# Performance work log

Hardware: AMD Instinct MI355X
Metric: run time of the kernel (lower is better)

Reference implementation:

```python
import jax, jax.numpy as jnp
import numpy as np

N = 100000; C = 128; H = 8; G = C // 4
B = 2; Z = 40; Y = 996; X = 996
WIN = 12; NUM_WIN = 200; EPS = 1e-3


def _make_indices():
    rng = np.random.RandomState(0)
    total = B * Z * Y * X
    uk = np.unique(rng.randint(0, total, size=300000).astype(np.int64))[:N]
    b = uk // (Z * Y * X); r = uk % (Z * Y * X)
    z = r // (Y * X); r = r % (Y * X)
    y = r // X; x = r % X
    return b, z, y, x, uk


def _neighbors(b, z, y, x, keys, offsets):
    # submanifold conv: output only at active sites; lookup coord+offset in active set
    sk = np.sort(keys); order = np.argsort(keys)
    cols = []
    for dz, dy, dx in offsets:
        nz, ny, nx = z + dz, y + dy, x + dx
        valid = (nz >= 0) & (nz < Z) & (ny >= 0) & (ny < Y) & (nx >= 0) & (nx < X)
        cand = ((b * Z + nz) * Y + ny) * X + nx
        pos = np.searchsorted(sk, cand)
        posc = np.minimum(pos, N - 1)
        found = valid & (sk[posc] == cand)
        cols.append(np.where(found, order[posc], N))  # N = sentinel (zero row)
    return np.stack(cols, axis=1).astype(np.int32)


def setup_inputs() -> dict:
    b, z, y, x, keys = _make_indices()
    off_k = [(dz, dy, dx) for dz in (-1, 0, 1) for dy in (-1, 0, 1) for dx in (-1, 0, 1)]
    off_h = [(0, 0, d) for d in range(-6, 7)]  # kernel (1,1,13) along x
    off_w = [(0, d, 0) for d in range(-6, 7)]  # kernel (1,13,1) along y
    nbr_k = _neighbors(b, z, y, x, keys, off_k)
    nbr_h = _neighbors(b, z, y, x, keys, off_h)
    nbr_w = _neighbors(b, z, y, x, keys, off_w)
    coords = np.stack([y, x], axis=0)
    wis = []
    for d in range(2):
        wkey = b * 1000 + coords[d] // WIN
        _, inv = np.unique(wkey, return_inverse=True)
        wis.append(inv)
    win_inds = np.stack(wis, 0).astype(np.int32)

    ks = jax.random.split(jax.random.key(0), 20)
    s = 0.05
    return dict(
        feats=jax.random.normal(ks[0], (N, C), jnp.float32),
        win_inds=jnp.asarray(win_inds),
        nbr_k=jnp.asarray(nbr_k), nbr_h=jnp.asarray(nbr_h), nbr_w=jnp.asarray(nbr_w),
        bn_g=jnp.ones((2, C)) + s * jax.random.normal(ks[1], (2, C)),
        bn_b=s * jax.random.normal(ks[2], (2, C)),
        Wqkv=s * jax.random.normal(ks[3], (2, C, 3 * C)),
        Wproj=s * jax.random.normal(ks[4], (2, C, C)),
        bproj=s * jax.random.normal(ks[5], (2, C)),
        bn1_g=jnp.ones((2, C)) + s * jax.random.normal(ks[6], (2, C)),
        bn1_b=s * jax.random.normal(ks[7], (2, C)),
        Wk=s * jax.random.normal(ks[8], (2, 27, G, G)),
        Wh=s * jax.random.normal(ks[9], (2, 13, G, G)),
        Ww=s * jax.random.normal(ks[10], (2, 13, G, G)),
        bn2_g=jnp.ones((2, C)) + s * jax.random.normal(ks[11], (2, C)),
        bn2_b=s * jax.random.normal(ks[12], (2, C)),
        fc1_W=s * jax.random.normal(ks[13], (2, C, 2 * C)),
        fc1_b=s * jax.random.normal(ks[14], (2, 2 * C)),
        fc2_W=s * jax.random.normal(ks[15], (2, 2 * C, C)),
        fc2_b=s * jax.random.normal(ks[16], (2, C)),
    )


def _bn(x, g, b):
    # BatchNorm1d, training-mode batch statistics, eps=1e-3
    m = jnp.mean(x, 0)
    v = jnp.var(x, 0)
    return (x - m) * jax.lax.rsqrt(v + EPS) * g + b


def _attn(x, wi, Wqkv, Wp, bp):
    # windowed linear attention: per-window K^T V + normalization by sum(K)
    q, k, v = jnp.split(x @ Wqkv, 3, axis=1)
    q = jax.nn.relu(q).reshape(N, H, C // H)
    k = jax.nn.relu(k).reshape(N, H, C // H)
    v = v.reshape(N, H, C // H)
    kv = jax.ops.segment_sum(jnp.einsum('nhc,nhd->nhcd', k, v), wi, NUM_WIN)
    s = jax.ops.segment_sum(k, wi, NUM_WIN)
    y = jnp.einsum('nhc,nhcd->nhd', q, kv[wi])
    z = jnp.sum(s[wi] * q, -1, keepdims=True)
    y = (y / (z + EPS)).reshape(N, C)
    return y @ Wp + bp


def _subm(f, nbr, W):
    # submanifold sparse conv via precomputed neighbor map (sentinel row = zeros)
    fp = jnp.concatenate([f, jnp.zeros((1, f.shape[1]), f.dtype)], 0)
    return jnp.einsum('nkc,kcd->nd', fp[nbr], W)


def reference(feats, win_inds, nbr_k, nbr_h, nbr_w, bn_g, bn_b, Wqkv, Wproj, bproj,
              bn1_g, bn1_b, Wk, Wh, Ww, bn2_g, bn2_b, fc1_W, fc1_b, fc2_W, fc2_b):
    f = feats
    for d in range(2):  # directions
        x = _attn(_bn(f, bn_g[d], bn_b[d]), win_inds[d], Wqkv[d], Wproj[d], bproj[d])
        f = f + x
        # CWI_FFN_Layer_3D
        fb = _bn(f, bn1_g[d], bn1_b[d])
        f2 = jnp.concatenate([
            _subm(fb[:, :G], nbr_k, Wk[d]),
            _subm(fb[:, G:2 * G], nbr_h, Wh[d]),
            _subm(fb[:, 2 * G:3 * G], nbr_w, Ww[d]),
            fb[:, 3 * G:],
        ], axis=1)
        f = fb + f2
        h = _bn(f, bn2_g[d], bn2_b[d])
        f = f + (jax.nn.relu(h @ fc1_W[d] + fc1_b[d]) @ fc2_W[d] + fc2_b[d])
    return f
```

## Files before the change

### kernel.cpp

```cpp
#include <hip/hip_runtime.h>
#include <math.h>

#define NPTS 100000
#define CCH 128
#define NWIN 200
#define NBLK_STATS 512
#define NBLK_SORT 391
#define SEGSZ 128
#define NSEG_MAX 1024

#define BM 128
#define BN 128
#define BK 64

typedef __attribute__((ext_vector_type(8))) short bf16x8;
typedef __attribute__((ext_vector_type(4))) float f32x4;
typedef __attribute__((ext_vector_type(4))) unsigned short u16x4;

__device__ __forceinline__ unsigned short f2bf(float f) {
    union { float f; unsigned u; } x; x.f = f;
    unsigned r = x.u + 0x7fff + ((x.u >> 16) & 1);
    return (unsigned short)(r >> 16);
}
__device__ __forceinline__ float bf2f(unsigned short h) {
    union { unsigned u; float f; } x; x.u = ((unsigned)h) << 16;
    return x.f;
}

__global__ __launch_bounds__(256) void bn_partial(const float* __restrict__ F,
                                                  float* __restrict__ part) {
    int t = threadIdx.x;
    int b = blockIdx.x;
    int rg = t >> 5;
    int c4 = (t & 31) * 4;
    float s0=0.f,s1=0.f,s2=0.f,s3=0.f,q0=0.f,q1=0.f,q2=0.f,q3=0.f;
    for (int n = b * 8 + rg; n < NPTS; n += NBLK_STATS * 8) {
        float4 v = *reinterpret_cast<const float4*>(&F[(size_t)n * CCH + c4]);
        s0 += v.x; s1 += v.y; s2 += v.z; s3 += v.w;
        q0 += v.x*v.x; q1 += v.y*v.y; q2 += v.z*v.z; q3 += v.w*v.w;
    }
    __shared__ float red[8][256];
    red[rg][c4+0] = s0; red[rg][c4+1] = s1; red[rg][c4+2] = s2; red[rg][c4+3] = s3;
    red[rg][128+c4+0] = q0; red[rg][128+c4+1] = q1; red[rg][128+c4+2] = q2; red[rg][128+c4+3] = q3;
    __syncthreads();
    float a = 0.f;
#pragma unroll
    for (int g = 0; g < 8; g++) a += red[g][t];
    part[b * 256 + t] = a;
}

__global__ __launch_bounds__(256) void bnred_k(const float* __restrict__ part,
                                               float* __restrict__ part2) {
    int t = threadIdx.x;
    int i = blockIdx.x;
    float a = 0.f;
#pragma unroll 8
    for (int j = 0; j < 32; j++) a += part[(size_t)(i * 32 + j) * 256 + t];
    part2[i * 256 + t] = a;
}

__global__ void bn_finalize(const float* __restrict__ part2,
                            const float* __restrict__ g, const float* __restrict__ bb,
                            float* __restrict__ scale, float* __restrict__ shift) {
    int c = threadIdx.x;
    double s = 0.0, q = 0.0;
#pragma unroll
    for (int b = 0; b < 16; b++) {
        s += (double)part2[b * 256 + c];
        q += (double)part2[b * 256 + 128 + c];
    }
    double m = s / (double)NPTS;
    double var = q / (double)NPTS - m * m;
    double rstd = 1.0 / sqrt(var + 1e-3);
    float sc = (float)rstd * g[c];
    scale[c] = sc;
    shift[c] = bb[c] - (float)m * sc;
}

__global__ __launch_bounds__(128) void wprep(
    const float* __restrict__ W, int K, int N,
    const float* __restrict__ sc, const float* __restrict__ sh,
    const float* __restrict__ bias,
    unsigned short* __restrict__ WT, float* __restrict__ biasf)
{
    int n = blockIdx.x;
    int t = threadIdx.x;
    float part = 0.f;
    for (int k = t; k < K; k += 128) {
        float w = W[(size_t)k * N + n];
        float s = sc ? sc[k] * w : w;
        WT[(size_t)n * K + k] = f2bf(s);
        if (sh) part += sh[k] * w;
    }
    __shared__ float red[128];
    red[t] = part;
    __syncthreads();
    for (int o = 64; o > 0; o >>= 1) {
        if (t < o) red[t] += red[t + o];
        __syncthreads();
    }
    if (t == 0) biasf[n] = red[0] + (bias ? bias[n] : 0.f);
}

__global__ void wconv_prep_all(const float* __restrict__ Wk, const float* __restrict__ Wh,
                               const float* __restrict__ Ww, unsigned short* __restrict__ WB) {
    int i = blockIdx.x * 256 + threadIdx.x;
    if (i >= 53 * 1024) return;
    int tap = i >> 10; int rem = i & 1023; int dd = rem >> 5; int c = rem & 31;
    const float* src; int lt;
    if (tap < 27)      { src = Wk; lt = tap; }
    else if (tap < 40) { src = Wh; lt = tap - 27; }
    else               { src = Ww; lt = tap - 40; }
    WB[i] = f2bf(src[lt * 1024 + c * 32 + dd]);
}

template<int NT>
__global__ __launch_bounds__(256) void gemm_knt(
    const float* __restrict__ A, int lda,
    const unsigned short* __restrict__ WT, const float* __restrict__ biasf,
    unsigned short* __restrict__ Out, int ldo, int reluLim)
{
    __shared__ __align__(16) char smem[49664];
    unsigned short* As = (unsigned short*)smem;
    unsigned short* Bs = (unsigned short*)(smem + 32768);
    float* Ep = (float*)(smem + 32768);

    const int tid  = threadIdx.x;
    const int wave = tid >> 6;
    const int lane = tid & 63;
    const int bm = blockIdx.x * BM;
    const int lrow = lane & 15;
    const int lhk  = lane >> 4;

#pragma unroll
    for (int pass = 0; pass < 16; pass++) {
        int row = pass * 8 + (tid >> 5);
        int grow = bm + row;
        int c4 = (tid & 31) * 4;
        float4 v = make_float4(0.f, 0.f, 0.f, 0.f);
        if (grow < NPTS)
            v = *reinterpret_cast<const float4*>(&A[(size_t)grow * lda + c4]);
        u16x4 h4 = { f2bf(v.x), f2bf(v.y), f2bf(v.z), f2bf(v.w) };
        int half = c4 >> 6;
        int cw = c4 & 63;
        int sw = (cw >> 3) ^ (row & 7);
        *reinterpret_cast<u16x4*>(&As[row * 128 + half * 64 + sw * 8 + (cw & 7)]) = h4;
    }

    for (int nt = 0; nt < NT; nt++) {
        const int bn = nt * BN;
        f32x4 acc[2][8];
#pragma unroll
        for (int i = 0; i < 2; i++)
#pragma unroll
            for (int j = 0; j < 8; j++)
                acc[i][j] = (f32x4){0.f, 0.f, 0.f, 0.f};

#pragma unroll
        for (int h = 0; h < 2; h++) {
            __syncthreads();
#pragma unroll
            for (int pass = 0; pass < 4; pass++) {
                int n = pass * 32 + (tid >> 3);
                bf16x8 w = *reinterpret_cast<const bf16x8*>(
                    &WT[(size_t)(bn + n) * 128 + h * 64 + (tid & 7) * 8]);
                int sw = (tid & 7) ^ (n & 7);
                *reinterpret_cast<bf16x8*>(&Bs[n * 64 + sw * 8]) = w;
            }
            __syncthreads();
#pragma unroll
            for (int ks = 0; ks < 2; ks++) {
                bf16x8 af[2], bfr[8];
#pragma unroll
                for (int fi = 0; fi < 2; fi++) {
                    int row = wave * 32 + fi * 16 + lrow;
                    int sw = (ks * 4 + lhk) ^ (row & 7);
                    af[fi] = *reinterpret_cast<const bf16x8*>(&As[row * 128 + h * 64 + sw * 8]);
                }
#pragma unroll
                for (int fj = 0; fj < 8; fj++) {
                    int col = fj * 16 + lrow;
                    int sw = (ks * 4 + lhk) ^ (col & 7);
                    bfr[fj] = *reinterpret_cast<const bf16x8*>(&Bs[col * 64 + sw * 8]);
                }
#pragma unroll
                for (int fi = 0; fi < 2; fi++)
#pragma unroll
                    for (int fj = 0; fj < 8; fj++)
                        acc[fi][fj] = __builtin_amdgcn_mfma_f32_16x16x32_bf16(
                            af[fi], bfr[fj], acc[fi][fj], 0, 0, 0);
            }
        }
        __syncthreads();

#pragma unroll
        for (int ch = 0; ch < 4; ch++) {
            if (wave == ch) {
#pragma unroll
                for (int fi = 0; fi < 2; fi++)
#pragma unroll
                    for (int fj = 0; fj < 8; fj++) {
                        int r0 = fi * 16 + lhk * 4;
                        int col = fj * 16 + lrow;
#pragma unroll
                        for (int r = 0; r < 4; r++)
                            Ep[(r0 + r) * 132 + col] = acc[fi][fj][r];
                    }
            }
            __syncthreads();
#pragma unroll
            for (int pass = 0; pass < 4; pass++) {
                int idx = pass * 256 + tid;
                int r = idx >> 5;
                int c4 = (idx & 31) * 4;
                int rr = bm + ch * 32 + r;
                if (rr < NPTS) {
                    float4 v = *reinterpret_cast<const float4*>(&Ep[r * 132 + c4]);
                    float4 b = *reinterpret_cast<const float4*>(&biasf[bn + c4]);
                    v.x += b.x; v.y += b.y; v.z += b.z; v.w += b.w;
                    int col = bn + c4;
                    if (col + 0 < reluLim) v.x = fmaxf(v.x, 0.f);
                    if (col + 1 < reluLim) v.y = fmaxf(v.y, 0.f);
                    if (col + 2 < reluLim) v.z = fmaxf(v.z, 0.f);
                    if (col + 3 < reluLim) v.w = fmaxf(v.w, 0.f);
                    u16x4 hv = { f2bf(v.x), f2bf(v.y), f2bf(v.z), f2bf(v.w) };
                    *reinterpret_cast<u16x4*>(&Out[(size_t)rr * ldo + bn + c4]) = hv;
                }
            }
            __syncthreads();
        }
    }
}

template<int ABF, int OBF>
__global__ __launch_bounds__(256) void gemm_t(
    const void* __restrict__ Ap, int lda,
    const unsigned short* __restrict__ WT, const float* __restrict__ biasf,
    int K,
    void* __restrict__ Outp, int ldo,
    int reluLim, int addFlag)
{
    __shared__ __align__(16) char smem[34048];
    unsigned short* As = (unsigned short*)smem;
    unsigned short* Bs = As + BM * BK;
    float* Ep = (float*)smem;

    const int tid  = threadIdx.x;
    const int wave = tid >> 6;
    const int lane = tid & 63;
    const int bm = blockIdx.y * BM;
    const int bn = blockIdx.x * BN;

    f32x4 acc[2][8];
#pragma unroll
    for (int i = 0; i < 2; i++)
#pragma unroll
        for (int j = 0; j < 8; j++)
            acc[i][j] = (f32x4){0.f, 0.f, 0.f, 0.f};

    const int lrow = lane & 15;
    const int lhk  = lane >> 4;

    for (int kk = 0; kk < K; kk += BK) {
        if (ABF) {
            const unsigned short* Ab = (const unsigned short*)Ap;
#pragma unroll
            for (int pass = 0; pass < 4; pass++) {
                int row = pass * 32 + (tid >> 3);
                int grow = bm + row;
                bf16x8 w = (bf16x8){0,0,0,0,0,0,0,0};
                if (grow < NPTS)
                    w = *reinterpret_cast<const bf16x8*>(&Ab[(size_t)grow * lda + kk + (tid & 7) * 8]);
                int sw = (tid & 7) ^ (row & 7);
                *reinterpret_cast<bf16x8*>(&As[row * 64 + sw * 8]) = w;
            }
        } else {
            const float* Af = (const float*)Ap;
            const int arow_t = tid >> 4;
            const int acol   = (tid & 15) * 4;
#pragma unroll
            for (int pass = 0; pass < 8; pass++) {
                int row = pass * 16 + arow_t;
                int grow = bm + row;
                float4 v = make_float4(0.f, 0.f, 0.f, 0.f);
                if (grow < NPTS)
                    v = *reinterpret_cast<const float4*>(&Af[(size_t)grow * lda + kk + acol]);
                u16x4 h = { f2bf(v.x), f2bf(v.y), f2bf(v.z), f2bf(v.w) };
                int s = acol >> 3;
                int sw = s ^ (row & 7);
                *reinterpret_cast<u16x4*>(&As[row * 64 + sw * 8 + (acol & 7)]) = h;
            }
        }
#pragma unroll
        for (int pass = 0; pass < 4; pass++) {
            int n = pass * 32 + (tid >> 3);
            bf16x8 w = *reinterpret_cast<const bf16x8*>(&WT[(size_t)(bn + n) * K + kk + (tid & 7) * 8]);
            int sw = (tid & 7) ^ (n & 7);
            *reinterpret_cast<bf16x8*>(&Bs[n * 64 + sw * 8]) = w;
        }
        __syncthreads();

#pragma unroll
        for (int ks = 0; ks < 2; ks++) {
            bf16x8 af[2], bfr[8];
#pragma unroll
            for (int fi = 0; fi < 2; fi++) {
                int row = wave * 32 + fi * 16 + lrow;
                int sw = (ks * 4 + lhk) ^ (row & 7);
                af[fi] = *reinterpret_cast<const bf16x8*>(&As[row * 64 + sw * 8]);
            }
#pragma unroll
            for (int fj = 0; fj < 8; fj++) {
                int col = fj * 16 + lrow;
                int sw = (ks * 4 + lhk) ^ (col & 7);
                bfr[fj] = *reinterpret_cast<const bf16x8*>(&Bs[col * 64 + sw * 8]);
            }
#pragma unroll
            for (int fi = 0; fi < 2; fi++)
#pragma unroll
                for (int fj = 0; fj < 8; fj++)
                    acc[fi][fj] = __builtin_amdgcn_mfma_f32_16x16x32_bf16(
                        af[fi], bfr[fj], acc[fi][fj], 0, 0, 0);
        }
        __syncthreads();
    }

    for (int hh = 0; hh < 2; hh++) {
        if ((wave >> 1) == hh) {
#pragma unroll
            for (int fi = 0; fi < 2; fi++) {
                int row = (wave & 1) * 32 + fi * 16 + (lane >> 4) * 4;
#pragma unroll
                for (int fj = 0; fj < 8; fj++) {
                    int col = fj * 16 + (lane & 15);
#pragma unroll
                    for (int r = 0; r < 4; r++)
                        Ep[(row + r) * 132 + col] = acc[fi][fj][r];
                }
            }
        }
        __syncthreads();
#pragma unroll
        for (int pass = 0; pass < 8; pass++) {
            int idx = pass * 256 + tid;
            int r = idx >> 5;
            int c4 = (idx & 31) * 4;
            int rr = bm + hh * 64 + r;
            if (rr < NPTS) {
                float4 v = *reinterpret_cast<const float4*>(&Ep[r * 132 + c4]);
                float4 b = *reinterpret_cast<const float4*>(&biasf[bn + c4]);
                v.x += b.x; v.y += b.y; v.z += b.z; v.w += b.w;
                int col = bn + c4;
                if (col + 0 < reluLim) v.x = fmaxf(v.x, 0.f);
                if (col + 1 < reluLim) v.y = fmaxf(v.y, 0.f);
                if (col + 2 < reluLim) v.z = fmaxf(v.z, 0.f);
                if (col + 3 < reluLim) v.w = fmaxf(v.w, 0.f);
                if (OBF) {
                    unsigned short* o = (unsigned short*)Outp + (size_t)rr * ldo + bn + c4;
                    u16x4 hv = { f2bf(v.x), f2bf(v.y), f2bf(v.z), f2bf(v.w) };
                    *reinterpret_cast<u16x4*>(o) = hv;
                } else {
                    float* o = (float*)Outp + (size_t)rr * ldo + bn + c4;
                    if (addFlag) {
                        float4 ov = *reinterpret_cast<const float4*>(o);
                        v.x += ov.x; v.y += ov.y; v.z += ov.z; v.w += ov.w;
                    }
                    *reinterpret_cast<float4*>(o) = v;
                }
            }
        }
        __syncthreads();
    }
}

__global__ __launch_bounds__(256) void hist2_k(const int* __restrict__ wi,
                                               int* __restrict__ BH) {
    __shared__ int h[NWIN];
    int t = threadIdx.x;
    if (t < NWIN) h[t] = 0;
    __syncthreads();
    int n = blockIdx.x * 256 + t;
    if (n < NPTS) atomicAdd(&h[wi[n]], 1);
    __syncthreads();
    if (t < NWIN) BH[blockIdx.x * 256 + t] = h[t];
}

__global__ __launch_bounds__(256) void colscan2_k(const int* __restrict__ BH,
                                                  int* __restrict__ OFFB,
                                                  int* __restrict__ TOT) {
    int w = blockIdx.x;
    int t = threadIdx.x;
    __shared__ int s[512];
    int v0 = (t < NBLK_SORT) ? BH[t * 256 + w] : 0;
    int v1 = (t + 256 < NBLK_SORT) ? BH[(t + 256) * 256 + w] : 0;
    s[t] = v0; s[t + 256] = v1;
    __syncthreads();
#pragma unroll
    for (int off = 1; off < 512; off <<= 1) {
        int a0 = (t >= off) ? s[t - off] : 0;
        int a1 = (t + 256 >= off) ? s[t + 256 - off] : 0;
        __syncthreads();
        s[t] += a0;
        s[t + 256] += a1;
        __syncthreads();
    }
    if (t < NBLK_SORT) OFFB[t * 256 + w] = s[t] - v0;
    if (t + 256 < NBLK_SORT) OFFB[(t + 256) * 256 + w] = s[t + 256] - v1;
    if (t == 0) TOT[w] = s[NBLK_SORT - 1];
}

__global__ __launch_bounds__(256) void meta2_k(const int* __restrict__ TOT,
                                               int* __restrict__ OFFS,
                                               int* __restrict__ SEGW, int* __restrict__ SEGP0,
                                               int* __restrict__ SEGP1, int* __restrict__ SEGBASE) {
    __shared__ int offs[NWIN + 1];
    __shared__ int segc[NWIN];
    int t = threadIdx.x;
    if (t < NWIN) segc[t] = TOT[t];
    __syncthreads();
    if (t == 0) {
        int a = 0;
        for (int w = 0; w < NWIN; w++) { int c = segc[w]; offs[w] = a; a += c; }
        offs[NWIN] = a;
    }
    __syncthreads();
    if (t <= NWIN) OFFS[t] = offs[t];
    if (t < NWIN) segc[t] = (offs[t + 1] - offs[t] + SEGSZ - 1) / SEGSZ;
    __syncthreads();
    if (t == 0) {
        int a = 0;
        for (int i = 0; i < NWIN; i++) { int c = segc[i]; segc[i] = a; SEGBASE[i] = a; a += c; }
        SEGBASE[NWIN] = a;
    }
    __syncthreads();
    if (t < NWIN) {
        int b = segc[t];
        int p0 = offs[t], p1 = offs[t + 1];
        for (int p = p0; p < p1; p += SEGSZ) {
            SEGW[b] = t; SEGP0[b] = p; SEGP1[b] = min(p + SEGSZ, p1); b++;
        }
    }
}

__global__ __launch_bounds__(256) void scatter2_k(const int* __restrict__ wi,
                                                  const int* __restrict__ OFFS,
                                                  const int* __restrict__ OFFB,
                                                  int* __restrict__ list) {
    __shared__ int h[NWIN];
    int t = threadIdx.x;
    if (t < NWIN) h[t] = 0;
    __syncthreads();
    int n = blockIdx.x * 256 + t;
    if (n < NPTS) {
        int w = wi[n];
        int r = atomicAdd(&h[w], 1);
        list[OFFS[w] + OFFB[blockIdx.x * 256 + w] + r] = n;
    }
}

__global__ __launch_bounds__(256) void window_kv_seg(
    const unsigned short* __restrict__ R0bf,
    const int* __restrict__ list,
    const int* __restrict__ SEGP0, const int* __restrict__ SEGP1,
    const int* __restrict__ SEGBASE,
    float* __restrict__ PKV)
{
    int sid = blockIdx.x;
    if (sid >= SEGBASE[NWIN]) return;
    int t = threadIdx.x;
    int p0 = SEGP0[sid], p1 = SEGP1[sid];
    __shared__ float buf[8][256];
    float acc[8] = {0.f,0.f,0.f,0.f,0.f,0.f,0.f,0.f};
    float sa = 0.f;
    int f0 = t * 8;
    int h = f0 >> 8;
    int c = (f0 >> 4) & 15;
    int d0 = f0 & 15;
    const int sr = t >> 5;
    const int c8 = (t & 31) * 8;

    for (int g = p0; g < p1; g += 8) {
        int m = min(8, p1 - g);
        int nj[8];
#pragma unroll
        for (int j = 0; j < 8; j++)
            nj[j] = list[(g + j < p1) ? g + j : p1 - 1];
        __syncthreads();
        {
            const unsigned short* row = &R0bf[(size_t)nj[sr] * 384 + 128];
            bf16x8 hv = *reinterpret_cast<const bf16x8*>(&row[c8]);
            float4 lo = make_float4(bf2f((unsigned short)hv[0]), bf2f((unsigned short)hv[1]),
                                    bf2f((unsigned short)hv[2]), bf2f((unsigned short)hv[3]));
            float4 hi = make_float4(bf2f((unsigned short)hv[4]), bf2f((unsigned short)hv[5]),
                                    bf2f((unsigned short)hv[6]), bf2f((unsigned short)hv[7]));
            *reinterpret_cast<float4*>(&buf[sr][c8]) = lo;
            *reinterpret_cast<float4*>(&buf[sr][c8 + 4]) = hi;
        }
        __syncthreads();
#pragma unroll
        for (int j = 0; j < 8; j++) {
            if (j >= m) break;
            float kc = buf[j][h * 16 + c];
#pragma unroll
            for (int i = 0; i < 8; i++) acc[i] += kc * buf[j][128 + h * 16 + d0 + i];
            if (t < 128) sa += buf[j][t];
        }
    }
    float* out = &PKV[(size_t)sid * 2176];
#pragma unroll
    for (int i = 0; i < 8; i++) out[f0 + i] = acc[i];
    if (t < 128) out[2048 + t] = sa;
}

__global__ __launch_bounds__(256) void kv_reduce(
    const float* __restrict__ PKV, const int* __restrict__ SEGBASE,
    float* __restrict__ KV, float* __restrict__ SB)
{
    int w = blockIdx.x;
    int t = threadIdx.x;
    int s0 = SEGBASE[w], s1 = SEGBASE[w + 1];
    float a[8] = {0.f,0.f,0.f,0.f,0.f,0.f,0.f,0.f};
    float sb = 0.f;
    for (int s = s0; s < s1; s++) {
        const float* p = &PKV[(size_t)s * 2176];
#pragma unroll
        for (int i = 0; i < 8; i++) a[i] += p[t * 8 + i];
        if (t < 128) sb += p[2048 + t];
    }
#pragma unroll
    for (int i = 0; i < 8; i++) KV[w * 2048 + t * 8 + i] = a[i];
    if (t < 128) SB[w * 128 + t] = sb;
}

__global__ __launch_bounds__(256) void attn_y_seg(
    const unsigned short* __restrict__ R0bf,
    unsigned short* __restrict__ Ybf,
    const int* __restrict__ list,
    const int* __restrict__ SEGW, const int* __restrict__ SEGP0,
    const int* __restrict__ SEGP1, const int* __restrict__ SEGBASE,
    const float* __restrict__ KV, const float* __restrict__ SB)
{
    int sid = blockIdx.x;
    if (sid >= SEGBASE[NWIN]) return;
    int t = threadIdx.x;
    int w = SEGW[sid];
    int g  = t >> 5;
    int h  = (t >> 2) & 7;
    int d4 = (t & 3) * 4;

    float4 kvr[16];
    const float* kvb = &KV[w * 2048 + h * 256 + d4];
#pragma unroll
    for (int cc = 0; cc < 16; cc++)
        kvr[cc] = *reinterpret_cast<const float4*>(&kvb[cc * 16]);
    float sreg[16];
    const float* sb = &SB[w * 128 + h * 16];
#pragma unroll
    for (int cc = 0; cc < 16; cc++) sreg[cc] = sb[cc];

    int p0 = SEGP0[sid], p1 = SEGP1[sid];
    for (int p = p0 + g; p < p1; p += 8) {
        int n = list[p];
        const unsigned short* q = &R0bf[(size_t)n * 384 + h * 16];
        bf16x8 qa = *reinterpret_cast<const bf16x8*>(&q[0]);
        bf16x8 qb = *reinterpret_cast<const bf16x8*>(&q[8]);
        float qq[16];
#pragma unroll
        for (int i = 0; i < 8; i++) {
            qq[i] = bf2f((unsigned short)qa[i]);
            qq[8 + i] = bf2f((unsigned short)qb[i]);
        }
        float z = 0.f;
        float4 y = make_float4(0.f, 0.f, 0.f, 0.f);
#pragma unroll
        for (int cc = 0; cc < 16; cc++) {
            z += qq[cc] * sreg[cc];
            y.x += qq[cc] * kvr[cc].x;
            y.y += qq[cc] * kvr[cc].y;
            y.z += qq[cc] * kvr[cc].z;
            y.w += qq[cc] * kvr[cc].w;
        }
        float inv = 1.f / (z + 1e-3f);
        u16x4 o = { f2bf(y.x * inv), f2bf(y.y * inv), f2bf(y.z * inv), f2bf(y.w * inv) };
        *reinterpret_cast<u16x4*>(&Ybf[(size_t)n * 128 + h * 16 + d4]) = o;
    }
}

__global__ void bn_apply(float* F, unsigned short* __restrict__ FBbf,
                         const float* __restrict__ scale, const float* __restrict__ shift)
{
    int i = blockIdx.x * 256 + threadIdx.x;
    int n = i >> 5;
    int c4 = (i & 31) * 4;
    float4 v = *reinterpret_cast<const float4*>(&F[n * CCH + c4]);
    float4 o;
    o.x = v.x * scale[c4 + 0] + shift[c4 + 0];
    o.y = v.y * scale[c4 + 1] + shift[c4 + 1];
    o.z = v.z * scale[c4 + 2] + shift[c4 + 2];
    o.w = v.w * scale[c4 + 3] + shift[c4 + 3];
    u16x4 hv = { f2bf(o.x), f2bf(o.y), f2bf(o.z), f2bf(o.w) };
    *reinterpret_cast<u16x4*>(&FBbf[(size_t)n * 128 + c4]) = hv;
    if (c4 >= 96) {
        float4 t = make_float4(2.f * o.x, 2.f * o.y, 2.f * o.z, 2.f * o.w);
        *reinterpret_cast<float4*>(&F[n * CCH + c4]) = t;
    }
}

__global__ __launch_bounds__(256) void conv_all(
    const int* __restrict__ nbr_k, const int* __restrict__ nbr_h, const int* __restrict__ nbr_w,
    const unsigned short* __restrict__ WBall,
    const unsigned short* __restrict__ FBbf,
    float* __restrict__ F)
{
    const int which = blockIdx.y;
    const int* nbr = (which == 0) ? nbr_k : (which == 1 ? nbr_h : nbr_w);
    const int kn = (which == 0) ? 27 : 13;
    const unsigned short* WB = WBall + ((which == 0) ? 0 : (which == 1 ? 27 * 1024 : 40 * 1024));
    const int off = which * 32;

    __shared__ __align__(16) char smem[18432];
    unsigned short* As = (unsigned short*)smem;
    float* Ep = (float*)smem;

    const int tid = threadIdx.x;
    const int wave = tid >> 6;
    const int lane = tid & 63;
    const int bm = blockIdx.x * 128;
    const int lrow = lane & 15;
    const int lk = lane >> 4;

    f32x4 acc[2][2];
#pragma unroll
    for (int i = 0; i < 2; i++)
#pragma unroll
        for (int j = 0; j < 2; j++)
            acc[i][j] = (f32x4){0.f, 0.f, 0.f, 0.f};

    const int r_st = tid >> 1;
    const int hf = tid & 1;
    const int grow = bm + r_st;
    const int* nb = nbr + (size_t)grow * kn;

    bf16x8 v0 = (bf16x8){0,0,0,0,0,0,0,0}, v1 = v0;
    {
        int idx = (grow < NPTS) ? nb[0] : NPTS;
        if (idx < NPTS) {
            const unsigned short* src = &FBbf[(size_t)idx * 128 + off];
            v0 = *reinterpret_cast<const bf16x8*>(&src[(hf * 2 + 0) * 8]);
            v1 = *reinterpret_cast<const bf16x8*>(&src[(hf * 2 + 1) * 8]);
        }
    }

    for (int k = 0; k < kn; k++) {
        __syncthreads();
        *reinterpret_cast<bf16x8*>(&As[r_st * 36 + (hf * 2 + 0) * 8]) = v0;
        *reinterpret_cast<bf16x8*>(&As[r_st * 36 + (hf * 2 + 1) * 8]) = v1;
        bf16x8 n0 = (bf16x8){0,0,0,0,0,0,0,0}, n1 = n0;
        if (k + 1 < kn) {
            int idx = (grow < NPTS) ? nb[k + 1] : NPTS;
            if (idx < NPTS) {
                const unsigned short* src = &FBbf[(size_t)idx * 128 + off];
                n0 = *reinterpret_cast<const bf16x8*>(&src[(hf * 2 + 0) * 8]);
                n1 = *reinterpret_cast<const bf16x8*>(&src[(hf * 2 + 1) * 8]);
            }
        }
        __syncthreads();
        bf16x8 af[2], bfr[2];
#pragma unroll
        for (int fi = 0; fi < 2; fi++) {
            int row = wave * 32 + fi * 16 + lrow;
            af[fi] = *reinterpret_cast<const bf16x8*>(&As[row * 36 + lk * 8]);
        }
#pragma unroll
        for (int fj = 0; fj < 2; fj++)
            bfr[fj] = *reinterpret_cast<const bf16x8*>(&WB[k * 1024 + (fj * 16 + lrow) * 32 + lk * 8]);
#pragma unroll
        for (int fi = 0; fi < 2; fi++)
#pragma unroll
            for (int fj = 0; fj < 2; fj++)
                acc[fi][fj] = __builtin_amdgcn_mfma_f32_16x16x32_bf16(
                    af[fi], bfr[fj], acc[fi][fj], 0, 0, 0);
        v0 = n0; v1 = n1;
    }

    __syncthreads();
#pragma unroll
    for (int fi = 0; fi < 2; fi++)
#pragma unroll
        for (int fj = 0; fj < 2; fj++) {
            int row0 = wave * 32 + fi * 16 + lk * 4;
            int col = fj * 16 + lrow;
#pragma unroll
            for (int r = 0; r < 4; r++)
                Ep[(row0 + r) * 36 + col] = acc[fi][fj][r];
        }
    __syncthreads();
#pragma unroll
    for (int pass = 0; pass < 4; pass++) {
        int idx = pass * 256 + tid;
        int r = idx >> 3;
        int c4 = (idx & 7) * 4;
        int rr = bm + r;
        if (rr < NPTS) {
            float4 v = *reinterpret_cast<const float4*>(&Ep[r * 36 + c4]);
            u16x4 fbh = *reinterpret_cast<const u16x4*>(&FBbf[(size_t)rr * 128 + off + c4]);
            v.x += bf2f(fbh.x); v.y += bf2f(fbh.y);
            v.z += bf2f(fbh.z); v.w += bf2f(fbh.w);
            *reinterpret_cast<float4*>(&F[(size_t)rr * CCH + off + c4]) = v;
        }
    }
}

extern "C" void kernel_launch(void* const* d_in, const int* in_sizes, int n_in,
                              void* d_out, int out_size, void* d_ws, size_t ws_size,
                              hipStream_t stream)
{
    const float* feats   = (const float*)d_in[0];
    const int*   win_inds= (const int*)d_in[1];
    const int*   nbr_k   = (const int*)d_in[2];
    const int*   nbr_h   = (const int*)d_in[3];
    const int*   nbr_w   = (const int*)d_in[4];
    const float* bn_g    = (const float*)d_in[5];
    const float* bn_b    = (const float*)d_in[6];
    const float* Wqkv    = (const float*)d_in[7];
    const float* Wproj   = (const float*)d_in[8];
    const float* bproj   = (const float*)d_in[9];
    const float* bn1_g   = (const float*)d_in[10];
    const float* bn1_b   = (const float*)d_in[11];
    const float* Wk      = (const float*)d_in[12];
    const float* Wh      = (const float*)d_in[13];
    const float* Ww      = (const float*)d_in[14];
    const float* bn2_g   = (const float*)d_in[15];
    const float* bn2_b   = (const float*)d_in[16];
    const float* fc1_W   = (const float*)d_in[17];
    const float* fc1_b   = (const float*)d_in[18];
    const float* fc2_W   = (const float*)d_in[19];
    const float* fc2_b   = (const float*)d_in[20];

    float* F  = (float*)d_out;
    float* KV = (float*)d_ws;
    float* SB = KV + NWIN * 2048;
    float* ST = SB + NWIN * 128;
    float* PART = ST + 768;
    float* PART2 = PART + NBLK_STATS * 256;
    float* PKV = PART2 + 16 * 256;
    int* OFFS = (int*)(PKV + (size_t)NSEG_MAX * 2176);
    int* TOT  = OFFS + 256;
    int* LIST = TOT + 256;
    int* BH   = LIST + 100096;
    int* OFFB = BH + NBLK_SORT * 256;
    int* SEGW = OFFB + NBLK_SORT * 256;
    int* SEGP0= SEGW + NSEG_MAX;
    int* SEGP1= SEGP0 + NSEG_MAX;
    int* SEGBASE = SEGP1 + NSEG_MAX;
    unsigned short* WQKVT = (unsigned short*)(SEGBASE + 256);
    unsigned short* WPROJT = WQKVT + 384 * 128;
    unsigned short* WFC1T  = WPROJT + 128 * 128;
    unsigned short* WFC2T  = WFC1T + 256 * 128;
    float* BQKV  = (float*)(WFC2T + 128 * 256);
    float* BPROJ = BQKV + 384;
    float* BFC1  = BPROJ + 128;
    float* BFC2  = BFC1 + 256;
    unsigned short* R0bf = (unsigned short*)(BFC2 + 128);
    unsigned short* Hbf  = R0bf;
    unsigned short* Ybf  = R0bf + (size_t)NPTS * 384;
    unsigned short* FBbf = Ybf + (size_t)NPTS * 128;
    unsigned short* WBall= FBbf + (size_t)NPTS * 128;

    hipMemcpyAsync(F, feats, (size_t)NPTS * CCH * sizeof(float),
                   hipMemcpyDeviceToDevice, stream);

    dim3 g1(1, 782);
    dim3 gc(782, 3);

    for (int d = 0; d < 2; d++) {
        const int* wi = win_inds + (size_t)d * NPTS;
        float* SC0 = ST, *SH0 = ST + 128, *SC1 = ST + 256, *SH1 = ST + 384,
             * SC2 = ST + 512, *SH2 = ST + 640;

        bn_partial<<<NBLK_STATS, 256, 0, stream>>>(F, PART);
        bnred_k<<<16, 256, 0, stream>>>(PART, PART2);
        bn_finalize<<<1, 128, 0, stream>>>(PART2, bn_g + d * CCH, bn_b + d * CCH, SC0, SH0);
        wprep<<<384, 128, 0, stream>>>(Wqkv + (size_t)d * CCH * 384, 128, 384,
                                       SC0, SH0, nullptr, WQKVT, BQKV);
        wprep<<<128, 128, 0, stream>>>(Wproj + (size_t)d * CCH * CCH, 128, 128,
                                       nullptr, nullptr, bproj + d * CCH, WPROJT, BPROJ);
        wconv_prep_all<<<212, 256, 0, stream>>>(Wk + (size_t)d * 27 * 1024,
                                                Wh + (size_t)d * 13 * 1024,
                                                Ww + (size_t)d * 13 * 1024, WBall);

        gemm_knt<3><<<782, 256, 0, stream>>>(F, CCH, WQKVT, BQKV, R0bf, 384, 256);

        hist2_k<<<NBLK_SORT, 256, 0, stream>>>(wi, BH);
        colscan2_k<<<NWIN, 256, 0, stream>>>(BH, OFFB, TOT);
        meta2_k<<<1, 256, 0, stream>>>(TOT, OFFS, SEGW, SEGP0, SEGP1, SEGBASE);
        scatter2_k<<<NBLK_SORT, 256, 0, stream>>>(wi, OFFS, OFFB, LIST);

        window_kv_seg<<<NSEG_MAX, 256, 0, stream>>>(R0bf, LIST, SEGP0, SEGP1, SEGBASE, PKV);
        kv_reduce<<<NWIN, 256, 0, stream>>>(PKV, SEGBASE, KV, SB);

        attn_y_seg<<<NSEG_MAX, 256, 0, stream>>>(R0bf, Ybf, LIST, SEGW, SEGP0, SEGP1,
                                                 SEGBASE, KV, SB);

        gemm_t<1,0><<<g1, 256, 0, stream>>>(Ybf, 128, WPROJT, BPROJ, 128,
                                            F, CCH, 0, 1);

        bn_partial<<<NBLK_STATS, 256, 0, stream>>>(F, PART);
        bnred_k<<<16, 256, 0, stream>>>(PART, PART2);
        bn_finalize<<<1, 128, 0, stream>>>(PART2, bn1_g + d * CCH, bn1_b + d * CCH, SC1, SH1);
        bn_apply<<<12500, 256, 0, stream>>>(F, FBbf, SC1, SH1);

        conv_all<<<gc, 256, 0, stream>>>(nbr_k, nbr_h, nbr_w, WBall, FBbf, F);

        bn_partial<<<NBLK_STATS, 256, 0, stream>>>(F, PART);
        bnred_k<<<16, 256, 0, stream>>>(PART, PART2);
        bn_finalize<<<1, 128, 0, stream>>>(PART2, bn2_g + d * CCH, bn2_b + d * CCH, SC2, SH2);
        wprep<<<256, 128, 0, stream>>>(fc1_W + (size_t)d * CCH * 256, 128, 256,
                                       SC2, SH2, fc1_b + d * 256, WFC1T, BFC1);
        wprep<<<128, 128, 0, stream>>>(fc2_W + (size_t)d * 256 * CCH, 256, 128,
                                       nullptr, nullptr, fc2_b + d * CCH, WFC2T, BFC2);

        gemm_knt<2><<<782, 256, 0, stream>>>(F, CCH, WFC1T, BFC1, Hbf, 256, 256);
        gemm_t<1,0><<<g1, 256, 0, stream>>>(Hbf, 256, WFC2T, BFC2, 256,
                                            F, CCH, 0, 1);
    }
}
```

Before: 793.7 us.

## Load conv gather operands directly into MFMA fragments, split conv by kernel size

The submanifold conv kernel stops staging gathered neighbour rows through shared memory with two barriers per tap. Each lane now loads its A fragment straight from global memory, with neighbour indices prefetched in chunks and the tap loop fully unrolled. The single 3-way launch becomes two templated launches, one for the 27-tap conv and one covering both 13-tap convs, so the tap count is a compile-time constant. This removes per-tap LDS traffic and synchronisation, but raises register pressure from the index arrays and issues more scattered global loads per lane.

```diff
diff --git a/kernel.cpp b/kernel.cpp
--- a/kernel.cpp
+++ b/kernel.cpp
@@ -606,21 +606,19 @@
     }
 }
 
-__global__ __launch_bounds__(256) void conv_all(
-    const int* __restrict__ nbr_k, const int* __restrict__ nbr_h, const int* __restrict__ nbr_w,
-    const unsigned short* __restrict__ WBall,
+template<int KN>
+__global__ __launch_bounds__(256) void conv_direct(
+    const int* __restrict__ nbrA, const int* __restrict__ nbrB,
+    const unsigned short* __restrict__ WBall, int wbBase,
     const unsigned short* __restrict__ FBbf,
-    float* __restrict__ F)
+    float* __restrict__ F, int offBase)
 {
     const int which = blockIdx.y;
-    const int* nbr = (which == 0) ? nbr_k : (which == 1 ? nbr_h : nbr_w);
-    const int kn = (which == 0) ? 27 : 13;
-    const unsigned short* WB = WBall + ((which == 0) ? 0 : (which == 1 ? 27 * 1024 : 40 * 1024));
-    const int off = which * 32;
-
-    __shared__ __align__(16) char smem[18432];
-    unsigned short* As = (unsigned short*)smem;
-    float* Ep = (float*)smem;
+    const int* __restrict__ nbr = which ? nbrB : nbrA;
+    const int off = offBase + which * 32;
+    const unsigned short* __restrict__ WB = WBall + wbBase + which * KN * 1024;
+
+    __shared__ __align__(16) float Ep[128 * 36];
 
     const int tid = threadIdx.x;
     const int wave = tid >> 6;
@@ -629,6 +627,9 @@
     const int lrow = lane & 15;
     const int lk = lane >> 4;
 
+    const int row0 = bm + wave * 32 + lrow;
+    const int row1 = row0 + 16;
+
     f32x4 acc[2][2];
 #pragma unroll
     for (int i = 0; i < 2; i++)
@@ -636,63 +637,41 @@
         for (int j = 0; j < 2; j++)
             acc[i][j] = (f32x4){0.f, 0.f, 0.f, 0.f};
 
-    const int r_st = tid >> 1;
-    const int hf = tid & 1;
-    const int grow = bm + r_st;
-    const int* nb = nbr + (size_t)grow * kn;
-
-    bf16x8 v0 = (bf16x8){0,0,0,0,0,0,0,0}, v1 = v0;
-    {
-        int idx = (grow < NPTS) ? nb[0] : NPTS;
-        if (idx < NPTS) {
-            const unsigned short* src = &FBbf[(size_t)idx * 128 + off];
-            v0 = *reinterpret_cast<const bf16x8*>(&src[(hf * 2 + 0) * 8]);
-            v1 = *reinterpret_cast<const bf16x8*>(&src[(hf * 2 + 1) * 8]);
-        }
-    }
-
-    for (int k = 0; k < kn; k++) {
-        __syncthreads();
-        *reinterpret_cast<bf16x8*>(&As[r_st * 36 + (hf * 2 + 0) * 8]) = v0;
-        *reinterpret_cast<bf16x8*>(&As[r_st * 36 + (hf * 2 + 1) * 8]) = v1;
-        bf16x8 n0 = (bf16x8){0,0,0,0,0,0,0,0}, n1 = n0;
-        if (k + 1 < kn) {
-            int idx = (grow < NPTS) ? nb[k + 1] : NPTS;
-            if (idx < NPTS) {
-                const unsigned short* src = &FBbf[(size_t)idx * 128 + off];
-                n0 = *reinterpret_cast<const bf16x8*>(&src[(hf * 2 + 0) * 8]);
-                n1 = *reinterpret_cast<const bf16x8*>(&src[(hf * 2 + 1) * 8]);
-            }
-        }
-        __syncthreads();
-        bf16x8 af[2], bfr[2];
-#pragma unroll
-        for (int fi = 0; fi < 2; fi++) {
-            int row = wave * 32 + fi * 16 + lrow;
-            af[fi] = *reinterpret_cast<const bf16x8*>(&As[row * 36 + lk * 8]);
-        }
-#pragma unroll
-        for (int fj = 0; fj < 2; fj++)
-            bfr[fj] = *reinterpret_cast<const bf16x8*>(&WB[k * 1024 + (fj * 16 + lrow) * 32 + lk * 8]);
-#pragma unroll
-        for (int fi = 0; fi < 2; fi++)
-#pragma unroll
-            for (int fj = 0; fj < 2; fj++)
-                acc[fi][fj] = __builtin_amdgcn_mfma_f32_16x16x32_bf16(
-                    af[fi], bfr[fj], acc[fi][fj], 0, 0, 0);
-        v0 = n0; v1 = n1;
-    }
-
-    __syncthreads();
+    constexpr int CHK = (KN == 27) ? 9 : 13;
+    for (int c0 = 0; c0 < KN; c0 += CHK) {
+        int i0[CHK], i1[CHK];
+#pragma unroll
+        for (int j = 0; j < CHK; j++) {
+            i0[j] = (row0 < NPTS) ? nbr[(size_t)row0 * KN + c0 + j] : NPTS;
+            i1[j] = (row1 < NPTS) ? nbr[(size_t)row1 * KN + c0 + j] : NPTS;
+        }
+#pragma unroll
+        for (int j = 0; j < CHK; j++) {
+            int k = c0 + j;
+            bf16x8 a0 = (bf16x8){0,0,0,0,0,0,0,0};
+            bf16x8 a1 = (bf16x8){0,0,0,0,0,0,0,0};
+            if (i0[j] < NPTS)
+                a0 = *reinterpret_cast<const bf16x8*>(&FBbf[(size_t)i0[j] * 128 + off + lk * 8]);
+            if (i1[j] < NPTS)
+                a1 = *reinterpret_cast<const bf16x8*>(&FBbf[(size_t)i1[j] * 128 + off + lk * 8]);
+            bf16x8 b0 = *reinterpret_cast<const bf16x8*>(&WB[k * 1024 + lrow * 32 + lk * 8]);
+            bf16x8 b1 = *reinterpret_cast<const bf16x8*>(&WB[k * 1024 + (16 + lrow) * 32 + lk * 8]);
+            acc[0][0] = __builtin_amdgcn_mfma_f32_16x16x32_bf16(a0, b0, acc[0][0], 0, 0, 0);
+            acc[0][1] = __builtin_amdgcn_mfma_f32_16x16x32_bf16(a0, b1, acc[0][1], 0, 0, 0);
+            acc[1][0] = __builtin_amdgcn_mfma_f32_16x16x32_bf16(a1, b0, acc[1][0], 0, 0, 0);
+            acc[1][1] = __builtin_amdgcn_mfma_f32_16x16x32_bf16(a1, b1, acc[1][1], 0, 0, 0);
+        }
+    }
+
 #pragma unroll
     for (int fi = 0; fi < 2; fi++)
 #pragma unroll
         for (int fj = 0; fj < 2; fj++) {
-            int row0 = wave * 32 + fi * 16 + lk * 4;
+            int r0 = wave * 32 + fi * 16 + lk * 4;
             int col = fj * 16 + lrow;
 #pragma unroll
             for (int r = 0; r < 4; r++)
-                Ep[(row0 + r) * 36 + col] = acc[fi][fj][r];
+                Ep[(r0 + r) * 36 + col] = acc[fi][fj][r];
         }
     __syncthreads();
 #pragma unroll
@@ -771,7 +750,7 @@
                    hipMemcpyDeviceToDevice, stream);
 
     dim3 g1(1, 782);
-    dim3 gc(782, 3);
+    dim3 gc13(782, 2);
 
     for (int d = 0; d < 2; d++) {
         const int* wi = win_inds + (size_t)d * NPTS;
@@ -810,7 +789,8 @@
         bn_finalize<<<1, 128, 0, stream>>>(PART2, bn1_g + d * CCH, bn1_b + d * CCH, SC1, SH1);
         bn_apply<<<12500, 256, 0, stream>>>(F, FBbf, SC1, SH1);
 
-        conv_all<<<gc, 256, 0, stream>>>(nbr_k, nbr_h, nbr_w, WBall, FBbf, F);
+        conv_direct<27><<<782, 256, 0, stream>>>(nbr_k, nbr_k, WBall, 0, FBbf, F, 0);
+        conv_direct<13><<<gc13, 256, 0, stream>>>(nbr_h, nbr_w, WBall, 27 * 1024, FBbf, F, 32);
 
         bn_partial<<<NBLK_STATS, 256, 0, stream>>>(F, PART);
         bnred_k<<<16, 256, 0, stream>>>(PART, PART2);
```

After: 724.7 us. -8.7%, faster.
